# Kernel tuning notes

Measured on AMD Instinct MI355X. Metric: run time of the kernel, lower is better.

The kernel has to match this reference:

```python
import jax, jax.numpy as jnp
import numpy as np


def sinusoidal_pe(S, D, dtype):
    # standard transformer sinusoidal positional encoding, shape [S, D]
    pos = jnp.arange(S, dtype=jnp.float32)[:, None]
    div = jnp.exp(jnp.arange(0, D, 2, dtype=jnp.float32) * (-np.log(10000.0) / D))
    ang = pos * div  # [S, D/2]
    pe = jnp.zeros((S, D), jnp.float32)
    pe = pe.at[:, 0::2].set(jnp.sin(ang)).at[:, 1::2].set(jnp.cos(ang))
    return pe.astype(dtype)


def setup_inputs() -> dict:
    key = jax.random.key(0)
    k1, k2, k3, k4, k5 = jax.random.split(key, 5)
    B, S, F, D, SEG = 64, 512, 64, 1024, 8
    x = jax.random.normal(k1, (B, S, F), jnp.float32)
    W_emb = jax.random.normal(k2, (F, D), jnp.float32) / np.sqrt(F)
    b_emb = jax.random.normal(k3, (D,), jnp.float32) * 0.01
    w_seg = jax.random.normal(k4, (SEG,), jnp.float32) / np.sqrt(SEG)
    b_seg = jax.random.normal(k5, (1,), jnp.float32) * 0.01
    return {"x": x, "W_emb": W_emb, "b_emb": b_emb, "w_seg": w_seg, "b_seg": b_seg}


def reference(x, W_emb, b_emb, w_seg, b_seg):
    B, S, F = x.shape
    D = W_emb.shape[1]
    seg_len = w_seg.shape[0]  # seq_len divisible by seg_len -> pad_len == 0 branch
    # input token embedding
    x1 = x @ W_emb + b_emb  # [B, S, D]
    # segment embedding: tensor_split at multiples of seg_len == reshape,
    # Linear(seg_len, 1) over the time axis of each chunk, broadcast over chunk.
    xr = x1.reshape(B, S // seg_len, seg_len, D)
    seg = jnp.einsum('bnsd,s->bnd', xr, w_seg) + b_seg[0]  # [B, n_seg, D]
    x2 = (xr + seg[:, :, None, :]).reshape(B, S, D)
    # positional encoding added to x2
    return x2 + sinusoidal_pe(S, D, x2.dtype)
```

## Files before the change

kernel.cpp:

```cpp
#include <hip/hip_runtime.h>
#include <stdint.h>


typedef __attribute__((ext_vector_type(8))) short short8;
typedef __attribute__((ext_vector_type(4))) float f32x4;

#define D_DIM 1024
#define WS_PE_OFF 131072
#define WS_X_OFF (131072 + 2097152)

__device__ __forceinline__ unsigned short f2bf(float f) {
  unsigned u = __float_as_uint(f);
  u = (u + 0x7FFFu + ((u >> 16) & 1u)) >> 16;
  return (unsigned short)u;
}

__global__ __launch_bounds__(256) void bert_setup_kernel(
    const float* __restrict__ x, const float* __restrict__ W,
    const float* __restrict__ b_emb, const float* __restrict__ w_seg,
    const float* __restrict__ b_seg, unsigned short* __restrict__ wsW,
    float* __restrict__ wsPE, unsigned short* __restrict__ wsX) {
  const int bid = blockIdx.x;
  const int tid = threadIdx.x;
  if (bid < 1024) {
    const int t = bid * 256 + tid;
    const float4* p = reinterpret_cast<const float4*>(x) + (size_t)t * 2;
    float4 v0 = p[0], v1 = p[1];
    short8 o;
    o[0] = (short)f2bf(v0.x); o[1] = (short)f2bf(v0.y);
    o[2] = (short)f2bf(v0.z); o[3] = (short)f2bf(v0.w);
    o[4] = (short)f2bf(v1.x); o[5] = (short)f2bf(v1.y);
    o[6] = (short)f2bf(v1.z); o[7] = (short)f2bf(v1.w);
    *reinterpret_cast<short8*>(wsX + (size_t)t * 8) = o;
  } else if (bid < 3072) {
    const int t = (bid - 1024) * 256 + tid;
    const int s = t >> 10;
    const int c = t & 1023;
    float Sw = 0.f;
#pragma unroll
    for (int i = 0; i < 8; ++i) Sw += w_seg[i];
    const float inv2pi = 0.15915494309189535f;
    const float KLOG = 0.02595256324130752f;
    float divrev = exp2f(-(float)(c >> 1) * KLOG) * inv2pi;
    float rev = (float)s * divrev + ((c & 1) ? 0.25f : 0.f);
    rev = rev - floorf(rev);
    float pe = __builtin_amdgcn_sinf(rev);
    wsPE[t] = pe + b_emb[c] * (1.f + Sw) + b_seg[0];
  } else {
    const int t = (bid - 3072) * 256 + tid;
    const int cf = t >> 7;
    const int kf = (t >> 6) & 1;
    const int lane = t & 63;
    const int col = cf * 16 + (lane & 15);
    const int k0 = kf * 32 + ((lane >> 4) << 3);
    short8 o;
#pragma unroll
    for (int i = 0; i < 8; ++i)
      o[i] = (short)f2bf(W[(size_t)(k0 + i) * D_DIM + col]);
    *reinterpret_cast<short8*>(wsW + (size_t)t * 8) = o;
  }
}

__global__ __launch_bounds__(256) void bert_main_kernel(
    const unsigned short* __restrict__ wsX,
    const unsigned short* __restrict__ wsW, const float* __restrict__ wsPE,
    const float* __restrict__ w_seg, float* __restrict__ out) {
  const int tid = threadIdx.x;
  const int lane = tid & 63;
  const int wave = tid >> 6;
  const int bid = blockIdx.x;
  const int nblk = (bid >> 3) & 7;
  const int mblk = (bid & 7) | ((bid >> 6) << 3);
  const int mbase = mblk * 64;
  const int nbase = nblk * 128;
  const int mw = wave >> 1;
  const int nw = wave & 1;
  const int L15 = lane & 15;
  const int g = lane >> 4;

  short8 aW[4][2];
#pragma unroll
  for (int cf = 0; cf < 4; ++cf) {
#pragma unroll
    for (int kf = 0; kf < 2; ++kf) {
      const int cfg = (nbase >> 4) + nw * 4 + cf;
      aW[cf][kf] = *reinterpret_cast<const short8*>(
          wsW + ((size_t)(cfg * 2 + kf) * 64 + lane) * 8);
    }
  }

  short8 bX[2][2];
#pragma unroll
  for (int rf = 0; rf < 2; ++rf) {
#pragma unroll
    for (int kf = 0; kf < 2; ++kf) {
      const int row = mbase + mw * 32 + rf * 16 + L15;
      bX[rf][kf] = *reinterpret_cast<const short8*>(
          wsX + (size_t)row * 64 + kf * 32 + g * 8);
    }
  }

  f32x4 acc[4][2];
#pragma unroll
  for (int cf = 0; cf < 4; ++cf) {
#pragma unroll
    for (int rf = 0; rf < 2; ++rf) {
      f32x4 c = {0.f, 0.f, 0.f, 0.f};
      c = __builtin_amdgcn_mfma_f32_16x16x32_bf16(aW[cf][0], bX[rf][0], c, 0,
                                                  0, 0);
      c = __builtin_amdgcn_mfma_f32_16x16x32_bf16(aW[cf][1], bX[rf][1], c, 0,
                                                  0, 0);
      acc[cf][rf] = c;
    }
  }

  const float t = w_seg[lane & 7];

#pragma unroll
  for (int cf = 0; cf < 4; ++cf) {
#pragma unroll
    for (int rf = 0; rf < 2; ++rf) {
      f32x4 a = acc[cf][rf];
      float q0 = a[0] * t, q1 = a[1] * t, q2 = a[2] * t, q3 = a[3] * t;
      q0 += __shfl_xor(q0, 1); q1 += __shfl_xor(q1, 1);
      q2 += __shfl_xor(q2, 1); q3 += __shfl_xor(q3, 1);
      q0 += __shfl_xor(q0, 2); q1 += __shfl_xor(q1, 2);
      q2 += __shfl_xor(q2, 2); q3 += __shfl_xor(q3, 2);
      q0 += __shfl_xor(q0, 4); q1 += __shfl_xor(q1, 4);
      q2 += __shfl_xor(q2, 4); q3 += __shfl_xor(q3, 4);

      const int row = mbase + mw * 32 + rf * 16 + L15;
      const int s = row & 511;
      const int colq = nbase + nw * 64 + cf * 16 + g * 4;
      const float4 pe4 =
          *reinterpret_cast<const float4*>(wsPE + (size_t)s * D_DIM + colq);
      float4 o;
      o.x = a[0] + q0 + pe4.x;
      o.y = a[1] + q1 + pe4.y;
      o.z = a[2] + q2 + pe4.z;
      o.w = a[3] + q3 + pe4.w;
      *reinterpret_cast<float4*>(out + (size_t)row * D_DIM + colq) = o;
    }
  }
}

extern "C" void kernel_launch(void* const* d_in, const int* in_sizes, int n_in,
                              void* d_out, int out_size, void* d_ws,
                              size_t ws_size, hipStream_t stream) {
  const float* x = (const float*)d_in[0];
  const float* W = (const float*)d_in[1];
  const float* b_emb = (const float*)d_in[2];
  const float* w_seg = (const float*)d_in[3];
  const float* b_seg = (const float*)d_in[4];
  float* out = (float*)d_out;

  unsigned short* wsW = (unsigned short*)d_ws;
  float* wsPE = (float*)((char*)d_ws + WS_PE_OFF);
  unsigned short* wsX = (unsigned short*)((char*)d_ws + WS_X_OFF);

  bert_setup_kernel<<<3104, 256, 0, stream>>>(x, W, b_emb, w_seg, b_seg, wsW,
                                              wsPE, wsX);
  bert_main_kernel<<<4096, 256, 0, stream>>>(wsX, wsW, wsPE, w_seg, out);
}
```

Measured before the change: 46.86 us.

## Compute positional encoding and bias inline in main kernel instead of workspace table

```diff
diff --git a/kernel.cpp b/kernel.cpp
--- a/kernel.cpp
+++ b/kernel.cpp
@@ -6,8 +6,7 @@
 typedef __attribute__((ext_vector_type(4))) float f32x4;
 
 #define D_DIM 1024
-#define WS_PE_OFF 131072
-#define WS_X_OFF (131072 + 2097152)
+#define WS_X_OFF 131072
 
 __device__ __forceinline__ unsigned short f2bf(float f) {
   unsigned u = __float_as_uint(f);
@@ -15,11 +14,9 @@
   return (unsigned short)u;
 }
 
-__global__ __launch_bounds__(256) void bert_setup_kernel(
+__global__ __launch_bounds__(256) void bert_setup(
     const float* __restrict__ x, const float* __restrict__ W,
-    const float* __restrict__ b_emb, const float* __restrict__ w_seg,
-    const float* __restrict__ b_seg, unsigned short* __restrict__ wsW,
-    float* __restrict__ wsPE, unsigned short* __restrict__ wsX) {
+    unsigned short* __restrict__ wsW, unsigned short* __restrict__ wsX) {
   const int bid = blockIdx.x;
   const int tid = threadIdx.x;
   if (bid < 1024) {
@@ -32,26 +29,12 @@
     o[4] = (short)f2bf(v1.x); o[5] = (short)f2bf(v1.y);
     o[6] = (short)f2bf(v1.z); o[7] = (short)f2bf(v1.w);
     *reinterpret_cast<short8*>(wsX + (size_t)t * 8) = o;
-  } else if (bid < 3072) {
+  } else {
     const int t = (bid - 1024) * 256 + tid;
-    const int s = t >> 10;
-    const int c = t & 1023;
-    float Sw = 0.f;
-#pragma unroll
-    for (int i = 0; i < 8; ++i) Sw += w_seg[i];
-    const float inv2pi = 0.15915494309189535f;
-    const float KLOG = 0.02595256324130752f;
-    float divrev = exp2f(-(float)(c >> 1) * KLOG) * inv2pi;
-    float rev = (float)s * divrev + ((c & 1) ? 0.25f : 0.f);
-    rev = rev - floorf(rev);
-    float pe = __builtin_amdgcn_sinf(rev);
-    wsPE[t] = pe + b_emb[c] * (1.f + Sw) + b_seg[0];
-  } else {
-    const int t = (bid - 3072) * 256 + tid;
-    const int cf = t >> 7;
+    const int cfg = t >> 7;
     const int kf = (t >> 6) & 1;
     const int lane = t & 63;
-    const int col = cf * 16 + (lane & 15);
+    const int col = cfg * 16 + (lane & 15);
     const int k0 = kf * 32 + ((lane >> 4) << 3);
     short8 o;
 #pragma unroll
@@ -61,10 +44,11 @@
   }
 }
 
-__global__ __launch_bounds__(256) void bert_main_kernel(
+__global__ __launch_bounds__(256) void bert_main(
     const unsigned short* __restrict__ wsX,
-    const unsigned short* __restrict__ wsW, const float* __restrict__ wsPE,
-    const float* __restrict__ w_seg, float* __restrict__ out) {
+    const unsigned short* __restrict__ wsW, const float* __restrict__ b_emb,
+    const float* __restrict__ w_seg, const float* __restrict__ b_seg,
+    float* __restrict__ out) {
   const int tid = threadIdx.x;
   const int lane = tid & 63;
   const int wave = tid >> 6;
@@ -80,48 +64,62 @@
 
   short8 aW[4][2];
 #pragma unroll
-  for (int cf = 0; cf < 4; ++cf) {
+  for (int cf = 0; cf < 4; ++cf)
 #pragma unroll
     for (int kf = 0; kf < 2; ++kf) {
       const int cfg = (nbase >> 4) + nw * 4 + cf;
       aW[cf][kf] = *reinterpret_cast<const short8*>(
           wsW + ((size_t)(cfg * 2 + kf) * 64 + lane) * 8);
     }
-  }
 
   short8 bX[2][2];
 #pragma unroll
-  for (int rf = 0; rf < 2; ++rf) {
+  for (int rf = 0; rf < 2; ++rf)
 #pragma unroll
     for (int kf = 0; kf < 2; ++kf) {
       const int row = mbase + mw * 32 + rf * 16 + L15;
       bX[rf][kf] = *reinterpret_cast<const short8*>(
           wsX + (size_t)row * 64 + kf * 32 + g * 8);
     }
-  }
 
   f32x4 acc[4][2];
 #pragma unroll
-  for (int cf = 0; cf < 4; ++cf) {
+  for (int cf = 0; cf < 4; ++cf)
 #pragma unroll
     for (int rf = 0; rf < 2; ++rf) {
       f32x4 c = {0.f, 0.f, 0.f, 0.f};
-      c = __builtin_amdgcn_mfma_f32_16x16x32_bf16(aW[cf][0], bX[rf][0], c, 0,
-                                                  0, 0);
-      c = __builtin_amdgcn_mfma_f32_16x16x32_bf16(aW[cf][1], bX[rf][1], c, 0,
-                                                  0, 0);
+      c = __builtin_amdgcn_mfma_f32_16x16x32_bf16(aW[cf][0], bX[rf][0], c, 0, 0, 0);
+      c = __builtin_amdgcn_mfma_f32_16x16x32_bf16(aW[cf][1], bX[rf][1], c, 0, 0, 0);
       acc[cf][rf] = c;
     }
+
+  float Sw = 0.f;
+#pragma unroll
+  for (int i = 0; i < 8; ++i) Sw += w_seg[i];
+  const float s1w = 1.f + Sw;
+  const float bseg = b_seg[0];
+  const float tseg = w_seg[lane & 7];
+
+  const float inv2pi = 0.15915494309189535f;
+  const float KLOG = 0.02595256324130752f;
+  float dv[4][2];
+#pragma unroll
+  for (int cf = 0; cf < 4; ++cf) {
+    const int p = (nbase + nw * 64 + cf * 16 + g * 4) >> 1;
+    dv[cf][0] = exp2f(-(float)p * KLOG) * inv2pi;
+    dv[cf][1] = exp2f(-(float)(p + 1) * KLOG) * inv2pi;
   }
-
-  const float t = w_seg[lane & 7];
 
 #pragma unroll
   for (int cf = 0; cf < 4; ++cf) {
+    const int colq = nbase + nw * 64 + cf * 16 + g * 4;
+    const float4 eb = *reinterpret_cast<const float4*>(b_emb + colq);
+    const float e0 = eb.x * s1w + bseg, e1 = eb.y * s1w + bseg;
+    const float e2 = eb.z * s1w + bseg, e3 = eb.w * s1w + bseg;
 #pragma unroll
     for (int rf = 0; rf < 2; ++rf) {
       f32x4 a = acc[cf][rf];
-      float q0 = a[0] * t, q1 = a[1] * t, q2 = a[2] * t, q3 = a[3] * t;
+      float q0 = a[0] * tseg, q1 = a[1] * tseg, q2 = a[2] * tseg, q3 = a[3] * tseg;
       q0 += __shfl_xor(q0, 1); q1 += __shfl_xor(q1, 1);
       q2 += __shfl_xor(q2, 1); q3 += __shfl_xor(q3, 1);
       q0 += __shfl_xor(q0, 2); q1 += __shfl_xor(q1, 2);
@@ -130,15 +128,17 @@
       q2 += __shfl_xor(q2, 4); q3 += __shfl_xor(q3, 4);
 
       const int row = mbase + mw * 32 + rf * 16 + L15;
-      const int s = row & 511;
-      const int colq = nbase + nw * 64 + cf * 16 + g * 4;
-      const float4 pe4 =
-          *reinterpret_cast<const float4*>(wsPE + (size_t)s * D_DIM + colq);
+      const float s = (float)(row & 511);
+      const float pe0 = __builtin_amdgcn_sinf(__builtin_amdgcn_fractf(s * dv[cf][0]));
+      const float pe1 = __builtin_amdgcn_sinf(__builtin_amdgcn_fractf(s * dv[cf][0] + 0.25f));
+      const float pe2 = __builtin_amdgcn_sinf(__builtin_amdgcn_fractf(s * dv[cf][1]));
+      const float pe3 = __builtin_amdgcn_sinf(__builtin_amdgcn_fractf(s * dv[cf][1] + 0.25f));
+
       float4 o;
-      o.x = a[0] + q0 + pe4.x;
-      o.y = a[1] + q1 + pe4.y;
-      o.z = a[2] + q2 + pe4.z;
-      o.w = a[3] + q3 + pe4.w;
+      o.x = a[0] + q0 + pe0 + e0;
+      o.y = a[1] + q1 + pe1 + e1;
+      o.z = a[2] + q2 + pe2 + e2;
+      o.w = a[3] + q3 + pe3 + e3;
       *reinterpret_cast<float4*>(out + (size_t)row * D_DIM + colq) = o;
     }
   }
@@ -155,10 +155,8 @@
   float* out = (float*)d_out;
 
   unsigned short* wsW = (unsigned short*)d_ws;
-  float* wsPE = (float*)((char*)d_ws + WS_PE_OFF);
   unsigned short* wsX = (unsigned short*)((char*)d_ws + WS_X_OFF);
 
-  bert_setup_kernel<<<3104, 256, 0, stream>>>(x, W, b_emb, w_seg, b_seg, wsW,
-                                              wsPE, wsX);
-  bert_main_kernel<<<4096, 256, 0, stream>>>(wsX, wsW, wsPE, w_seg, out);
+  bert_setup<<<1056, 256, 0, stream>>>(x, W, wsW, wsX);
+  bert_main<<<4096, 256, 0, stream>>>(wsX, wsW, b_emb, w_seg, b_seg, out);
 }
```

After: 39.38 us. 1.19x faster.
